# Optimization experiments

Hardware: AMD Instinct MI355X
Metric: run time of the kernel (lower is better)

The kernel has to match this reference:

```python
import jax, jax.numpy as jnp
import numpy as np

DIM, DIM_K, DIM_U, HEADS, SCOPE = 256, 16, 1, 4, 23
DIM_V = DIM // HEADS  # 64
EPS = 1e-5


def _bn(x, gamma, beta):
    # training-mode BatchNorm2d over (b, h, w), biased variance, per-channel affine
    mean = jnp.mean(x, axis=(0, 2, 3), keepdims=True)
    var = jnp.var(x, axis=(0, 2, 3), keepdims=True)
    xhat = (x - mean) * jax.lax.rsqrt(var + EPS)
    return xhat * gamma[None, :, None, None] + beta[None, :, None, None]


def setup_inputs() -> dict:
    key = jax.random.key(0)
    ks = jax.random.split(key, 8)
    c_out = HEADS * DIM_K + DIM_K * DIM_U + DIM_V * DIM_U  # 144
    x = jax.random.normal(ks[0], (16, DIM, 64, 64), dtype=jnp.float32)
    w_qkv = jax.random.normal(ks[1], (c_out, DIM), dtype=jnp.float32) * (1.0 / np.sqrt(DIM))
    gamma_q = jnp.ones((HEADS * DIM_K,), jnp.float32)
    beta_q = jnp.zeros((HEADS * DIM_K,), jnp.float32)
    gamma_v = jnp.ones((DIM_V * DIM_U,), jnp.float32)
    beta_v = jnp.zeros((DIM_V * DIM_U,), jnp.float32)
    fan_in = DIM_U * SCOPE * SCOPE
    w_lconv = jax.random.normal(ks[2], (DIM_K, DIM_U, 1, SCOPE, SCOPE), dtype=jnp.float32) * (1.0 / np.sqrt(fan_in))
    b_lconv = jnp.zeros((DIM_K,), jnp.float32)
    return {"x": x, "w_qkv": w_qkv, "gamma_q": gamma_q, "beta_q": beta_q,
            "gamma_v": gamma_v, "beta_v": beta_v, "w_lconv": w_lconv, "b_lconv": b_lconv}


def reference(x, w_qkv, gamma_q, beta_q, gamma_v, beta_v, w_lconv, b_lconv):
    b, c, h, w = x.shape
    m = h * w
    # 1x1 conv projection
    qkv = jnp.einsum('oc,bchw->bohw', w_qkv, x)
    q = qkv[:, :HEADS * DIM_K]
    k = qkv[:, HEADS * DIM_K:HEADS * DIM_K + DIM_K * DIM_U]
    v = qkv[:, HEADS * DIM_K + DIM_K * DIM_U:]
    # q: 'b (k n) h w -> b n k m'
    q = _bn(q, gamma_q, beta_q).reshape(b, DIM_K, HEADS, m).transpose(0, 2, 1, 3)
    # v: 'b (v u) h w -> b u v m'
    v = _bn(v, gamma_v, beta_v).reshape(b, DIM_V, DIM_U, m).transpose(0, 2, 1, 3)
    # k: 'b (u k) h w -> b u k m', softmax over m
    k = jax.nn.softmax(k.reshape(b, DIM_U, DIM_K, m), axis=-1)
    content_lambda = jnp.einsum('bukm,buvm->bkv', k, v)
    # position lambda: Conv3d over (v, h, w) with kernel (1, scope, scope)
    v5 = v.reshape(b, DIM_U, DIM_V, h, w)
    pad = (SCOPE - 1) // 2
    pl = jax.lax.conv_general_dilated(
        v5, w_lconv, window_strides=(1, 1, 1),
        padding=[(0, 0), (pad, pad), (pad, pad)],
        dimension_numbers=('NCDHW', 'OIDHW', 'NCDHW'))
    pl = pl + b_lconv[None, :, None, None, None]
    position_lambda = pl.reshape(b, DIM_K, DIM_V, m)
    content_output = jnp.einsum('bnkm,bkv->bnvm', q, content_lambda)
    position_output = jnp.einsum('bnkm,bkvm->bnvm', q, position_lambda)
    out = (content_output + position_output).reshape(b, HEADS * DIM_V, h, w)
    return out
```

## Files before the change

kernel.cpp:

```cpp
#include <hip/hip_runtime.h>
#include <math.h>

#define NB    16
#define CDIM  256
#define COUT  144
#define MPIX  4096
#define SCOPE 23
#define PADH  11
#define BNEPS 1e-5f

typedef __attribute__((ext_vector_type(4))) float f32x4;
typedef __attribute__((ext_vector_type(8))) short s16x8;

__device__ __forceinline__ unsigned short f2bf(float f) {
    unsigned u = __builtin_bit_cast(unsigned, f);
    unsigned r = (u + 0x7FFFu + ((u >> 16) & 1u)) >> 16;
    return (unsigned short)r;
}

__global__ void prep_frags(const float* __restrict__ w, const float* __restrict__ wl,
                           short* __restrict__ wqf, short* __restrict__ wfrag) {
    int i = blockIdx.x * 256 + threadIdx.x;
    if (i < 36864) {
        int j = i & 7, lane = (i >> 3) & 63;
        int fi = i >> 9;
        int mf = fi % 9, kc = fi / 9;
        int o = mf * 16 + (lane & 15);
        int c = kc * 32 + (lane >> 4) * 8 + j;
        wqf[i] = (short)f2bf(w[o * 256 + c]);
        return;
    }
    int i2 = i - 36864;
    if (i2 < 23 * 64 * 8) {
        int j = i2 & 7, l = (i2 >> 3) & 63, dy = i2 >> 9;
        int k = l & 15, t = ((l >> 4) << 3) + j;
        float wv = (t < SCOPE) ? wl[k * 529 + dy * 23 + t] : 0.f;
        wfrag[i2] = (short)f2bf(wv);
    }
}

__global__ void __launch_bounds__(256, 4) gemm_qkv(const float* __restrict__ x,
                                                   const short* __restrict__ wqf,
                                                   float* __restrict__ qkv,
                                                   float* __restrict__ statpart) {
    __shared__ unsigned pk[16 * 65];
    __shared__ float ssum[4][144], ssq[4][144];
    int mt = blockIdx.x, b = blockIdx.y;
    int m0 = mt * 64;
    int tid = threadIdx.x;
    int px64 = tid & 63, c2b = tid >> 6;
    int lane = tid & 63, wv = tid >> 6;
    int pxl = lane & 15, kgq = lane >> 4;
    const float* xb = x + (size_t)b * CDIM * MPIX;
    float* qtb = qkv + (size_t)b * COUT * MPIX;
    const s16x8* wfv = (const s16x8*)wqf;

    f32x4 acc[9];
#pragma unroll
    for (int mf = 0; mf < 9; mf++) acc[mf] = 0.f;

#pragma unroll 1
    for (int kc = 0; kc < 8; kc++) {
        if (kc > 0) __syncthreads();
#pragma unroll
        for (int it = 0; it < 4; it++) {
            int c2 = c2b + it * 4;
            float x0 = xb[(size_t)(kc * 32 + 2 * c2) * MPIX + m0 + px64];
            float x1 = xb[(size_t)(kc * 32 + 2 * c2 + 1) * MPIX + m0 + px64];
            pk[c2 * 65 + px64] = (unsigned)f2bf(x0) | ((unsigned)f2bf(x1) << 16);
        }
        __syncthreads();
        const unsigned* bp = &pk[kgq * 4 * 65 + wv * 16 + pxl];
        int4 bi = make_int4(bp[0], bp[65], bp[130], bp[195]);
        s16x8 bf = __builtin_bit_cast(s16x8, bi);
#pragma unroll
        for (int mf = 0; mf < 9; mf++) {
            s16x8 af = wfv[(kc * 9 + mf) * 64 + lane];
            acc[mf] = __builtin_amdgcn_mfma_f32_16x16x32_bf16(af, bf, acc[mf], 0, 0, 0);
        }
    }

    int m = m0 + wv * 16 + pxl;
#pragma unroll
    for (int mf = 0; mf < 9; mf++) {
#pragma unroll
        for (int r = 0; r < 4; r++) {
            int o = mf * 16 + kgq * 4 + r;
            if (mf < 4) qtb[(size_t)m * 64 + o] = acc[mf][r];
            else qkv[((size_t)b * COUT + o) * MPIX + m] = acc[mf][r];
        }
    }

#pragma unroll
    for (int mf = 0; mf < 9; mf++) {
#pragma unroll
        for (int r = 0; r < 4; r++) {
            float s = acc[mf][r];
            float s2 = s * s;
#pragma unroll
            for (int off = 1; off < 16; off <<= 1) {
                s += __shfl_xor(s, off);
                s2 += __shfl_xor(s2, off);
            }
            if (pxl == 0) {
                int ch = mf * 16 + kgq * 4 + r;
                ssum[wv][ch] = s;
                ssq[wv][ch] = s2;
            }
        }
    }
    __syncthreads();
    if (tid < 144) {
        float s = ssum[0][tid] + ssum[1][tid] + ssum[2][tid] + ssum[3][tid];
        float s2 = ssq[0][tid] + ssq[1][tid] + ssq[2][tid] + ssq[3][tid];
        size_t idx = (((size_t)tid * 16 + b) * 64 + mt) * 2;
        statpart[idx + 0] = s;
        statpart[idx + 1] = s2;
    }
}

__global__ void stats_finalize(const float* __restrict__ statpart,
                               const float* __restrict__ gq, const float* __restrict__ bq,
                               const float* __restrict__ gv, const float* __restrict__ bv,
                               float* __restrict__ ascale, float* __restrict__ dshift) {
    int sch = blockIdx.x;
    int gch = (sch < 64) ? sch : sch + 16;
    const float* sp = statpart + (size_t)gch * 1024 * 2;
    int tid = threadIdx.x;
    float s = 0.f, s2 = 0.f;
    for (int i = tid; i < 1024; i += 256) {
        s += sp[i * 2 + 0];
        s2 += sp[i * 2 + 1];
    }
#pragma unroll
    for (int off = 32; off > 0; off >>= 1) {
        s += __shfl_down(s, off);
        s2 += __shfl_down(s2, off);
    }
    __shared__ float red[8];
    int wid = tid >> 6, lane = tid & 63;
    if (lane == 0) { red[wid * 2] = s; red[wid * 2 + 1] = s2; }
    __syncthreads();
    if (tid == 0) {
        float ts = 0.f, ts2 = 0.f;
#pragma unroll
        for (int w2 = 0; w2 < 4; w2++) { ts += red[w2 * 2]; ts2 += red[w2 * 2 + 1]; }
        const float invN = 1.0f / 65536.0f;
        float mean = ts * invN;
        float var = ts2 * invN - mean * mean;
        float g = (sch < 64) ? gq[sch] : gv[sch - 64];
        float be = (sch < 64) ? bq[sch] : bv[sch - 64];
        float a = g * rsqrtf(var + BNEPS);
        ascale[sch] = a;
        dshift[sch] = be - mean * a;
    }
}

__global__ void softmax_k(const float* __restrict__ qkv, float* __restrict__ p) {
    int bk = blockIdx.x;
    int b = bk >> 4, kc = bk & 15;
    const float* row = qkv + ((size_t)b * COUT + 64 + kc) * MPIX;
    int tid = threadIdx.x;
    float v[16];
    float mx = -INFINITY;
#pragma unroll
    for (int i = 0; i < 16; i++) {
        v[i] = row[tid + i * 256];
        mx = fmaxf(mx, v[i]);
    }
#pragma unroll
    for (int off = 32; off > 0; off >>= 1) mx = fmaxf(mx, __shfl_down(mx, off));
    __shared__ float redm[4];
    __shared__ float bm;
    int wid = tid >> 6, lane = tid & 63;
    if (lane == 0) redm[wid] = mx;
    __syncthreads();
    if (tid == 0) bm = fmaxf(fmaxf(redm[0], redm[1]), fmaxf(redm[2], redm[3]));
    __syncthreads();
    mx = bm;
    float s = 0.f;
#pragma unroll
    for (int i = 0; i < 16; i++) {
        v[i] = expf(v[i] - mx);
        s += v[i];
    }
#pragma unroll
    for (int off = 32; off > 0; off >>= 1) s += __shfl_down(s, off);
    __shared__ float reds[4];
    __shared__ float bs;
    if (lane == 0) reds[wid] = s;
    __syncthreads();
    if (tid == 0) bs = reds[0] + reds[1] + reds[2] + reds[3];
    __syncthreads();
    float r = 1.0f / bs;
    float* prow = p + ((size_t)b * 16 + kc) * MPIX;
#pragma unroll
    for (int i = 0; i < 16; i++) prow[tid + i * 256] = v[i] * r;
}

__global__ void cl_partial(const float* __restrict__ qkv, const float* __restrict__ p,
                           const float* __restrict__ ascale, const float* __restrict__ dshift,
                           float* __restrict__ clpart) {
    __shared__ float vsT[128][65];
    int mc = blockIdx.x, b = blockIdx.y;
    int m0 = mc * 256;
    int tid = threadIdx.x;
    int vc = tid & 63, kg = tid >> 6;
    float acc[4] = {0.f, 0.f, 0.f, 0.f};
    for (int half = 0; half < 2; half++) {
        int mh = m0 + half * 128;
        __syncthreads();
        for (int i = tid; i < 64 * 128; i += 256) {
            int r = i >> 7, c = i & 127;
            vsT[c][r] = fmaf(ascale[64 + r], qkv[((size_t)b * COUT + 80 + r) * MPIX + mh + c],
                             dshift[64 + r]);
        }
        __syncthreads();
        for (int mm = 0; mm < 128; mm++) {
            float vv = vsT[mm][vc];
#pragma unroll
            for (int i = 0; i < 4; i++) {
                int kc = kg * 4 + i;
                acc[i] = fmaf(p[((size_t)b * 16 + kc) * MPIX + mh + mm], vv, acc[i]);
            }
        }
    }
#pragma unroll
    for (int i = 0; i < 4; i++) {
        int kc = kg * 4 + i;
        clpart[(((size_t)b * 16 + mc) * 16 + kc) * 64 + vc] = acc[i];
    }
}

__global__ void cl_reduce(const float* __restrict__ clpart, float* __restrict__ cl) {
    int b = blockIdx.x;
    for (int o = threadIdx.x; o < 1024; o += 256) {
        float s = 0.f;
        for (int mc = 0; mc < 16; mc++)
            s += clpart[((size_t)b * 16 + mc) * 1024 + o];
        cl[(size_t)b * 1024 + o] = s;
    }
}

__global__ void __launch_bounds__(256) bnq_t(float* __restrict__ qkv,
                                             const float* __restrict__ ascale,
                                             const float* __restrict__ dshift) {
    __shared__ float sv[64][65];
    int mt = blockIdx.x, b = blockIdx.y;
    int m0 = mt * 64;
    float* qb = qkv + (size_t)b * COUT * MPIX;
    int tid = threadIdx.x;
    int c = tid & 63, mg = tid >> 6;
    float a = ascale[c], d = dshift[c];
#pragma unroll
    for (int i = 0; i < 16; i++) {
        int m = mg * 16 + i;
        sv[m][c] = fmaf(a, qb[(size_t)(m0 + m) * 64 + c], d);
    }
    __syncthreads();
    int m = tid >> 2, jb = (tid & 3) * 8;
    unsigned dw[8];
#pragma unroll
    for (int j = 0; j < 8; j++) {
        int cc = jb * 2 + 2 * j;
        dw[j] = (unsigned)f2bf(sv[m][cc]) | ((unsigned)f2bf(sv[m][cc + 1]) << 16);
    }
    unsigned* dst = (unsigned*)qb + (size_t)(m0 + m) * 64 + jb;
    *(uint4*)dst = make_uint4(dw[0], dw[1], dw[2], dw[3]);
    *(uint4*)(dst + 4) = make_uint4(dw[4], dw[5], dw[6], dw[7]);
}

#define SPW 88
#define LD_FRAG(P) __builtin_bit_cast(s16x8, make_int4((P)[0], (P)[2], (P)[4], (P)[6]))
#define STEP(DY, J) do {                                                        \
    const unsigned* pnew_ = xbase + ((DY) + 3) * SPW;                           \
    rw[((J) + 3) & 3][0] = LD_FRAG(pnew_);                                      \
    rw[((J) + 3) & 3][1] = LD_FRAG(pnew_ + 16);                                 \
    int dyn_ = ((DY) + 3 < 22) ? (DY) + 3 : 22;                                 \
    wr[((J) + 3) & 3] = wf[dyn_ * 64 + lane];                                   \
    _Pragma("unroll")                                                           \
    for (int ty_ = 0; ty_ < 4; ty_++) {                                         \
      _Pragma("unroll")                                                         \
      for (int x2_ = 0; x2_ < 2; x2_++) {                                       \
        int t_ = ty_ * 2 + x2_;                                                 \
        acc[t_] = __builtin_amdgcn_mfma_f32_16x16x32_bf16(                      \
            wr[(J) & 3], rw[((J) + ty_) & 3][x2_], acc[t_], 0, 0, 0);           \
      }                                                                         \
    }                                                                           \
  } while (0)

__global__ void __launch_bounds__(256, 4) lambda_main(
    const float* __restrict__ qkv, const float* __restrict__ ascale,
    const float* __restrict__ dshift, const float* __restrict__ cl,
    const short* __restrict__ wfrag, const float* __restrict__ bl,
    float* __restrict__ out) {
    __shared__ unsigned spack[54 * SPW + 8];
    __shared__ float sck[16];

    int vc = blockIdx.x, b = blockIdx.y, h = blockIdx.z;
    int tid = threadIdx.x;

    if (tid < 16) sck[tid] = cl[((size_t)b * 16 + tid) * 64 + vc] + bl[tid];

    float av = ascale[64 + vc], dv = dshift[64 + vc];
    const float* vrow = qkv + ((size_t)b * COUT + 80 + vc) * MPIX;
    for (int i = tid; i < 54 * SPW; i += 256) {
        int y = i / SPW, e = i - y * SPW;
        int iy = h * 32 + y - PADH;
        float f0 = 0.f, f1 = 0.f;
        if ((unsigned)iy < 64u) {
            int ix0 = e - PADH, ix1 = e - PADH + 1;
            if ((unsigned)ix0 < 64u) f0 = fmaf(av, vrow[iy * 64 + ix0], dv);
            if ((unsigned)ix1 < 64u) f1 = fmaf(av, vrow[iy * 64 + ix1], dv);
        }
        spack[i] = (unsigned)f2bf(f0) | ((unsigned)f2bf(f1) << 16);
    }
    if (tid < 8) spack[54 * SPW + tid] = 0u;
    __syncthreads();

    int lane = tid & 63;
    int wv = tid >> 6;
    int px = lane & 15;
    int kg = lane >> 4;
    const s16x8* wf = (const s16x8*)wfrag;

    const unsigned* qtb = (const unsigned*)(qkv + (size_t)b * COUT * MPIX);
    float* ob = out + (size_t)b * 256 * MPIX;

    float sck_l[4];
#pragma unroll
    for (int r = 0; r < 4; r++) sck_l[r] = sck[kg * 4 + r];

#pragma unroll 1
    for (int gg = 0; gg < 2; gg++) {
        int y0 = (gg * 4 + wv) * 4;
        const unsigned* base = &spack[y0 * SPW + px + kg * 8];

#pragma unroll 1
        for (int xh = 0; xh < 2; xh++) {
            const unsigned* xbase = base + xh * 32;
            f32x4 acc[8];
#pragma unroll
            for (int t = 0; t < 8; t++) acc[t] = 0.f;

            s16x8 rw[4][2];
            s16x8 wr[4];
#pragma unroll
            for (int r0 = 0; r0 < 3; r0++) {
                const unsigned* p = xbase + r0 * SPW;
                rw[r0][0] = LD_FRAG(p);
                rw[r0][1] = LD_FRAG(p + 16);
            }
#pragma unroll
            for (int s = 0; s < 3; s++) wr[s] = wf[s * 64 + lane];

#pragma unroll 1
            for (int i8 = 0; i8 < 2; i8++) {
                int dyb = i8 * 8;
                STEP(dyb + 0, 0);
                STEP(dyb + 1, 1);
                STEP(dyb + 2, 2);
                STEP(dyb + 3, 3);
                STEP(dyb + 4, 4);
                STEP(dyb + 5, 5);
                STEP(dyb + 6, 6);
                STEP(dyb + 7, 7);
            }
            STEP(16, 0);
            STEP(17, 1);
            STEP(18, 2);
            STEP(19, 3);
            STEP(20, 4);
            STEP(21, 5);
            STEP(22, 6);

#pragma unroll
            for (int t = 0; t < 8; t++) {
                int ty = t >> 1, x2 = t & 1;
                int m0 = (h * 32 + y0 + ty) * 64 + (xh * 2 + x2) * 16;
                float lam[4];
#pragma unroll
                for (int r = 0; r < 4; r++) lam[r] = acc[t][r] + sck_l[r];
                const unsigned* qp = &qtb[(size_t)(m0 + px) * 64 + kg * 8];
                uint4 qa = *(const uint4*)qp;
                uint4 qb4 = *(const uint4*)(qp + 4);
                unsigned dws[8] = {qa.x, qa.y, qa.z, qa.w, qb4.x, qb4.y, qb4.z, qb4.w};
                float po[4] = {0.f, 0.f, 0.f, 0.f};
#pragma unroll
                for (int d = 0; d < 8; d++) {
                    float q0 = __builtin_bit_cast(float, dws[d] << 16);
                    float q1 = __builtin_bit_cast(float, dws[d] & 0xffff0000u);
                    int i0 = 2 * d, i1 = 2 * d + 1;
                    po[i0 & 3] = fmaf(q0, lam[i0 >> 2], po[i0 & 3]);
                    po[i1 & 3] = fmaf(q1, lam[i1 >> 2], po[i1 & 3]);
                }
#pragma unroll
                for (int n = 0; n < 4; n++) {
                    po[n] += __shfl_xor(po[n], 16);
                    po[n] += __shfl_xor(po[n], 32);
                }
                float sv = (kg == 0) ? po[0] : (kg == 1) ? po[1] : (kg == 2) ? po[2] : po[3];
                ob[(size_t)(kg * 64 + vc) * MPIX + m0 + px] = sv;
            }
        }
    }
}

extern "C" void kernel_launch(void* const* d_in, const int* in_sizes, int n_in,
                              void* d_out, int out_size, void* d_ws, size_t ws_size,
                              hipStream_t stream) {
    const float* x      = (const float*)d_in[0];
    const float* w_qkv  = (const float*)d_in[1];
    const float* gq     = (const float*)d_in[2];
    const float* bq     = (const float*)d_in[3];
    const float* gv     = (const float*)d_in[4];
    const float* bv     = (const float*)d_in[5];
    const float* wl     = (const float*)d_in[6];
    const float* bl     = (const float*)d_in[7];
    float* out = (float*)d_out;

    float* ws     = (float*)d_ws;
    float* qkv    = ws;
    float* p      = qkv + 9437184;
    float* ascale = p + 1048576;
    float* dshift = ascale + 128;
    float* clpart = dshift + 128;
    float* clb    = clpart + 262144;
    short* wfrag  = (short*)(clb + 16384);
    short* wqf    = (short*)(clb + 16384 + 5888 + 64);
    float* statpart = (float*)(wqf + 36864);

    prep_frags<<<190, 256, 0, stream>>>(w_qkv, wl, wqf, wfrag);
    gemm_qkv<<<dim3(64, 16), 256, 0, stream>>>(x, wqf, qkv, statpart);
    stats_finalize<<<128, 256, 0, stream>>>(statpart, gq, bq, gv, bv, ascale, dshift);
    softmax_k<<<256, 256, 0, stream>>>(qkv, p);
    cl_partial<<<dim3(16, 16), 256, 0, stream>>>(qkv, p, ascale, dshift, clpart);
    cl_reduce<<<16, 256, 0, stream>>>(clpart, clb);
    bnq_t<<<dim3(64, 16), 256, 0, stream>>>(qkv, ascale, dshift);
    lambda_main<<<dim3(64, 16, 2), 256, 0, stream>>>(qkv, ascale, dshift, clb, wfrag, bl, out);
}
```

Measured before the change: 202.1 us.

## Fuse softmax exp-sum into GEMM epilogue and drop separate softmax kernel

The GEMM epilogue now computes per-tile sums of exp(k) and writes partials, which stats_finalize reduces into per-row reciprocal denominators. cl_partial recomputes exp(k) times that reciprocal on the fly into shared memory instead of reading a precomputed probability buffer. This removes the softmax_k kernel and its 4 MB write and read. The price is skipping max subtraction, which risks overflow for large logits, plus extra exp work in the GEMM and cl_partial.

```diff
diff --git a/kernel.cpp b/kernel.cpp
--- a/kernel.cpp
+++ b/kernel.cpp
@@ -42,9 +42,11 @@
 __global__ void __launch_bounds__(256, 4) gemm_qkv(const float* __restrict__ x,
                                                    const short* __restrict__ wqf,
                                                    float* __restrict__ qkv,
-                                                   float* __restrict__ statpart) {
+                                                   float* __restrict__ statpart,
+                                                   float* __restrict__ kpart) {
     __shared__ unsigned pk[16 * 65];
     __shared__ float ssum[4][144], ssq[4][144];
+    __shared__ float sse[4][16];
     int mt = blockIdx.x, b = blockIdx.y;
     int m0 = mt * 64;
     int tid = threadIdx.x;
@@ -102,6 +104,12 @@
                 s += __shfl_xor(s, off);
                 s2 += __shfl_xor(s2, off);
             }
+            if (mf == 4) {
+                float e = __expf(acc[mf][r]);
+#pragma unroll
+                for (int off = 1; off < 16; off <<= 1) e += __shfl_xor(e, off);
+                if (pxl == 0) sse[wv][kgq * 4 + r] = e;
+            }
             if (pxl == 0) {
                 int ch = mf * 16 + kgq * 4 + r;
                 ssum[wv][ch] = s;
@@ -117,16 +125,33 @@
         statpart[idx + 0] = s;
         statpart[idx + 1] = s2;
     }
+    if (tid >= 144 && tid < 160) {
+        int kc = tid - 144;
+        float e = sse[0][kc] + sse[1][kc] + sse[2][kc] + sse[3][kc];
+        kpart[((size_t)kc * 16 + b) * 64 + mt] = e;
+    }
 }
 
 __global__ void stats_finalize(const float* __restrict__ statpart,
+                               const float* __restrict__ kpart,
                                const float* __restrict__ gq, const float* __restrict__ bq,
                                const float* __restrict__ gv, const float* __restrict__ bv,
-                               float* __restrict__ ascale, float* __restrict__ dshift) {
+                               float* __restrict__ ascale, float* __restrict__ dshift,
+                               float* __restrict__ ksm) {
+    int tid = threadIdx.x;
+    if (blockIdx.x >= 128) {
+        int id = blockIdx.x - 128;
+        if (tid < 64) {
+            float s = kpart[(size_t)id * 64 + tid];
+#pragma unroll
+            for (int off = 32; off > 0; off >>= 1) s += __shfl_down(s, off);
+            if (tid == 0) ksm[id] = 1.0f / s;
+        }
+        return;
+    }
     int sch = blockIdx.x;
     int gch = (sch < 64) ? sch : sch + 16;
     const float* sp = statpart + (size_t)gch * 1024 * 2;
-    int tid = threadIdx.x;
     float s = 0.f, s2 = 0.f;
     for (int i = tid; i < 1024; i += 256) {
         s += sp[i * 2 + 0];
@@ -156,56 +181,17 @@
     }
 }
 
-__global__ void softmax_k(const float* __restrict__ qkv, float* __restrict__ p) {
-    int bk = blockIdx.x;
-    int b = bk >> 4, kc = bk & 15;
-    const float* row = qkv + ((size_t)b * COUT + 64 + kc) * MPIX;
-    int tid = threadIdx.x;
-    float v[16];
-    float mx = -INFINITY;
-#pragma unroll
-    for (int i = 0; i < 16; i++) {
-        v[i] = row[tid + i * 256];
-        mx = fmaxf(mx, v[i]);
-    }
-#pragma unroll
-    for (int off = 32; off > 0; off >>= 1) mx = fmaxf(mx, __shfl_down(mx, off));
-    __shared__ float redm[4];
-    __shared__ float bm;
-    int wid = tid >> 6, lane = tid & 63;
-    if (lane == 0) redm[wid] = mx;
-    __syncthreads();
-    if (tid == 0) bm = fmaxf(fmaxf(redm[0], redm[1]), fmaxf(redm[2], redm[3]));
-    __syncthreads();
-    mx = bm;
-    float s = 0.f;
-#pragma unroll
-    for (int i = 0; i < 16; i++) {
-        v[i] = expf(v[i] - mx);
-        s += v[i];
-    }
-#pragma unroll
-    for (int off = 32; off > 0; off >>= 1) s += __shfl_down(s, off);
-    __shared__ float reds[4];
-    __shared__ float bs;
-    if (lane == 0) reds[wid] = s;
-    __syncthreads();
-    if (tid == 0) bs = reds[0] + reds[1] + reds[2] + reds[3];
-    __syncthreads();
-    float r = 1.0f / bs;
-    float* prow = p + ((size_t)b * 16 + kc) * MPIX;
-#pragma unroll
-    for (int i = 0; i < 16; i++) prow[tid + i * 256] = v[i] * r;
-}
-
-__global__ void cl_partial(const float* __restrict__ qkv, const float* __restrict__ p,
+__global__ void cl_partial(const float* __restrict__ qkv, const float* __restrict__ ksm,
                            const float* __restrict__ ascale, const float* __restrict__ dshift,
                            float* __restrict__ clpart) {
     __shared__ float vsT[128][65];
+    __shared__ float pk2[16][132];
+    __shared__ float skr[16];
     int mc = blockIdx.x, b = blockIdx.y;
     int m0 = mc * 256;
     int tid = threadIdx.x;
     int vc = tid & 63, kg = tid >> 6;
+    if (tid < 16) skr[tid] = ksm[(size_t)tid * 16 + b];
     float acc[4] = {0.f, 0.f, 0.f, 0.f};
     for (int half = 0; half < 2; half++) {
         int mh = m0 + half * 128;
@@ -215,13 +201,17 @@
             vsT[c][r] = fmaf(ascale[64 + r], qkv[((size_t)b * COUT + 80 + r) * MPIX + mh + c],
                              dshift[64 + r]);
         }
+        for (int i = tid; i < 16 * 128; i += 256) {
+            int kc = i >> 7, mm = i & 127;
+            pk2[kc][mm] = __expf(qkv[((size_t)b * COUT + 64 + kc) * MPIX + mh + mm]) * skr[kc];
+        }
         __syncthreads();
         for (int mm = 0; mm < 128; mm++) {
             float vv = vsT[mm][vc];
 #pragma unroll
             for (int i = 0; i < 4; i++) {
                 int kc = kg * 4 + i;
-                acc[i] = fmaf(p[((size_t)b * 16 + kc) * MPIX + mh + mm], vv, acc[i]);
+                acc[i] = fmaf(pk2[kc][mm], vv, acc[i]);
             }
         }
     }
@@ -421,20 +411,21 @@
 
     float* ws     = (float*)d_ws;
     float* qkv    = ws;
-    float* p      = qkv + 9437184;
-    float* ascale = p + 1048576;
+    float* ascale = qkv + 9437184;
     float* dshift = ascale + 128;
     float* clpart = dshift + 128;
     float* clb    = clpart + 262144;
     short* wfrag  = (short*)(clb + 16384);
     short* wqf    = (short*)(clb + 16384 + 5888 + 64);
     float* statpart = (float*)(wqf + 36864);
+    float* kpart  = statpart + 294912;
+    float* ksm    = kpart + 16384;
 
     prep_frags<<<190, 256, 0, stream>>>(w_qkv, wl, wqf, wfrag);
-    gemm_qkv<<<dim3(64, 16), 256, 0, stream>>>(x, wqf, qkv, statpart);
-    stats_finalize<<<128, 256, 0, stream>>>(statpart, gq, bq, gv, bv, ascale, dshift);
-    softmax_k<<<256, 256, 0, stream>>>(qkv, p);
-    cl_partial<<<dim3(16, 16), 256, 0, stream>>>(qkv, p, ascale, dshift, clpart);
+    gemm_qkv<<<dim3(64, 16), 256, 0, stream>>>(x, wqf, qkv, statpart, kpart);
+    stats_finalize<<<384, 256, 0, stream>>>(statpart, kpart, gq, bq, gv, bv,
+                                            ascale, dshift, ksm);
+    cl_partial<<<dim3(16, 16), 256, 0, stream>>>(qkv, ksm, ascale, dshift, clpart);
     cl_reduce<<<16, 256, 0, stream>>>(clpart, clb);
     bnq_t<<<dim3(64, 16), 256, 0, stream>>>(qkv, ascale, dshift);
     lambda_main<<<dim3(64, 16, 2), 256, 0, stream>>>(qkv, ascale, dshift, clb, wfrag, bl, out);
```

Result: no change. 200.6 us (-0.7%).
